# Kernel tuning notes

Hardware: AMD Instinct MI355X
Metric: run time of the kernel (lower is better)

## Reference

```python
import jax, jax.numpy as jnp
import numpy as np

# Standard TCN TemporalBlock (Bai et al.): dilated causal conv -> chomp -> relu ->
# (dropout, identity at eval) x2, plus 1x1-conv residual, final relu.
# PyTorch pads (k-1)*d on both sides then chomps the right, which equals
# left-only causal padding of (k-1)*d.

def _causal_conv(x, w, b, dilation):
    pad = (w.shape[-1] - 1) * dilation
    y = jax.lax.conv_general_dilated(
        x, w, window_strides=(1,), padding=[(pad, 0)],
        rhs_dilation=(dilation,), dimension_numbers=('NCH', 'OIH', 'NCH'))
    return y + b[None, :, None]

def _block(x, w1, b1, w2, b2, wd, bd, dil):
    h = jax.nn.relu(_causal_conv(x, w1, b1, dil))
    h = jax.nn.relu(_causal_conv(h, w2, b2, dil))
    res = _causal_conv(x, wd, bd, 1)  # 1x1 downsample (channel counts differ)
    return jax.nn.relu(h + res)

def setup_inputs() -> dict:
    key = jax.random.key(0)
    ks = jax.random.split(key, 18)
    B, Cin, L, C1, C2, H, K, O = 4096, 30, 256, 100, 200, 8, 5, 1
    def rn(k, shape, s=0.05):
        return jax.random.normal(k, shape, dtype=jnp.float32) * s
    return {
        'x': rn(ks[0], (B, Cin, L), 1.0),
        'task_labels': jax.random.randint(ks[1], (B,), 0, H),
        # TCN level 0: in_features -> 100, dilation 1
        'w1_0': rn(ks[2], (C1, Cin, K)), 'b1_0': rn(ks[3], (C1,)),
        'w2_0': rn(ks[4], (C1, C1, K)),  'b2_0': rn(ks[5], (C1,)),
        'wd_0': rn(ks[6], (C1, Cin, 1)), 'bd_0': rn(ks[7], (C1,)),
        # TCN level 1: 100 -> 200, dilation 2
        'w1_1': rn(ks[8], (C2, C1, K)),  'b1_1': rn(ks[9], (C2,)),
        'w2_1': rn(ks[10], (C2, C2, K)), 'b2_1': rn(ks[11], (C2,)),
        'wd_1': rn(ks[12], (C2, C1, 1)), 'bd_1': rn(ks[13], (C2,)),
        # 8 per-task heads, stacked: Linear(200->100), Tanh, Linear(100->1)
        'hw1': rn(ks[14], (H, C1, C2)), 'hb1': rn(ks[15], (H, C1)),
        'hw2': rn(ks[16], (H, O, C1)),  'hb2': rn(ks[17], (H, O)),
    }

def reference(x, task_labels, w1_0, b1_0, w2_0, b2_0, wd_0, bd_0,
              w1_1, b1_1, w2_1, b2_1, wd_1, bd_1, hw1, hb1, hw2, hb2):
    # TCN backbone (eval mode: dropout is identity)
    y = _block(x, w1_0, b1_0, w2_0, b2_0, wd_0, bd_0, 1)
    y = _block(y, w1_1, b1_1, w2_1, b2_1, wd_1, bd_1, 2)
    feat = y[:, :, -1]  # [B, 200] last timestep
    # Vectorized per-task head dispatch: gather each sample's head weights.
    # Mathematically identical to the per-task gather/MLP/scatter loop.
    W1 = hw1[task_labels]  # [B, 100, 200]
    B1 = hb1[task_labels]  # [B, 100]
    W2 = hw2[task_labels]  # [B, 1, 100]
    B2 = hb2[task_labels]  # [B, 1]
    h = jnp.tanh(jnp.einsum('bd,bod->bo', feat, W1) + B1)
    return jnp.einsum('bo,bpo->bp', h, W2) + B2  # [B, 1]
```

## Files before the change

kernel.cpp:

```cpp
#include <hip/hip_runtime.h>
#include <math.h>


#define B_TOT 4096
#define CIN   30
#define LSEQ  256
#define C1    100
#define C2    200
#define KW    5
#define T0    231
#define WIN   25
#define NT_H0 21
#define NT_Y0 9
#define NT_H1 5

#define NB1 4
__global__ __launch_bounds__(256) void k_h0(const float* __restrict__ x,
                                            const float* __restrict__ w1,
                                            const float* __restrict__ b1,
                                            float* __restrict__ h0) {
  __shared__ float xs[NB1 * CIN * WIN];
  const int b0 = blockIdx.x * NB1;
  const int tid = threadIdx.x;
  for (int idx = tid; idx < NB1 * CIN * WIN; idx += 256) {
    int b = idx / (CIN * WIN);
    int r = idx - b * (CIN * WIN);
    int ci = r / WIN;
    int u = r - ci * WIN;
    xs[idx] = x[(size_t)(b0 + b) * (CIN * LSEQ) + ci * LSEQ + T0 + u];
  }
  __syncthreads();
  const int bl = tid & (NB1 - 1);
  const int cg = tid >> 2;
  const float* xb = xs + bl * (CIN * WIN);
  const int c0 = cg;
  const bool has2 = (cg < C1 - 64);
  const int c1 = has2 ? cg + 64 : cg;

  float acc0[NT_H0], acc1[NT_H0];
  const float bias0 = b1[c0], bias1 = b1[c1];
#pragma unroll
  for (int i = 0; i < NT_H0; ++i) { acc0[i] = bias0; acc1[i] = bias1; }
  const float* wr0 = w1 + c0 * (CIN * KW);
  const float* wr1 = w1 + c1 * (CIN * KW);
  for (int ci = 0; ci < CIN; ++ci) {
    float xr[WIN];
#pragma unroll
    for (int u = 0; u < WIN; ++u) xr[u] = xb[ci * WIN + u];
#pragma unroll
    for (int k = 0; k < KW; ++k) {
      const float wa = wr0[ci * KW + k];
      const float wb = wr1[ci * KW + k];
#pragma unroll
      for (int i = 0; i < NT_H0; ++i) {
        acc0[i] = fmaf(xr[i + k], wa, acc0[i]);
        acc1[i] = fmaf(xr[i + k], wb, acc1[i]);
      }
    }
  }
  float* o0 = h0 + (size_t)(b0 + bl) * (C1 * NT_H0) + c0 * NT_H0;
#pragma unroll
  for (int i = 0; i < NT_H0; ++i) o0[i] = fmaxf(acc0[i], 0.f);
  if (has2) {
    float* o1 = h0 + (size_t)(b0 + bl) * (C1 * NT_H0) + c1 * NT_H0;
#pragma unroll
    for (int i = 0; i < NT_H0; ++i) o1[i] = fmaxf(acc1[i], 0.f);
  }
}

#define NB2 4
__global__ __launch_bounds__(256) void k_y0(const float* __restrict__ x,
                                            const float* __restrict__ h0,
                                            const float* __restrict__ w2,
                                            const float* __restrict__ b2,
                                            const float* __restrict__ wd,
                                            const float* __restrict__ bd,
                                            float* __restrict__ y0) {
  __shared__ float hs[NB2 * C1 * NT_H0];
  __shared__ float xrs[NB2 * CIN * NT_Y0];
  const int b0 = blockIdx.x * NB2;
  const int tid = threadIdx.x;
  for (int idx = tid; idx < NB2 * C1 * NT_H0; idx += 256) {
    int b = idx / (C1 * NT_H0);
    int r = idx - b * (C1 * NT_H0);
    hs[idx] = h0[(size_t)(b0 + b) * (C1 * NT_H0) + r];
  }
  for (int idx = tid; idx < NB2 * CIN * NT_Y0; idx += 256) {
    int b = idx / (CIN * NT_Y0);
    int r = idx - b * (CIN * NT_Y0);
    int ci = r / NT_Y0;
    int j = r - ci * NT_Y0;
    xrs[idx] = x[(size_t)(b0 + b) * (CIN * LSEQ) + ci * LSEQ + T0 + 8 + 2 * j];
  }
  __syncthreads();
  const int bl = tid & (NB2 - 1);
  const int cg = tid >> 2;
  const float* hb = hs + bl * (C1 * NT_H0);
  const float* xb = xrs + bl * (CIN * NT_Y0);
  const int c0 = cg;
  const bool has2 = (cg < C1 - 64);
  const int c1 = has2 ? cg + 64 : cg;

  float acc0[NT_Y0], acc1[NT_Y0];
  const float bA = b2[c0], bB = b2[c1];
#pragma unroll
  for (int j = 0; j < NT_Y0; ++j) { acc0[j] = bA; acc1[j] = bB; }
  const float* wr0 = w2 + c0 * (C1 * KW);
  const float* wr1 = w2 + c1 * (C1 * KW);
  for (int ci = 0; ci < C1; ++ci) {
    float hr[NT_H0];
#pragma unroll
    for (int u = 0; u < NT_H0; ++u) hr[u] = hb[ci * NT_H0 + u];
#pragma unroll
    for (int k = 0; k < KW; ++k) {
      const float wa = wr0[ci * KW + k];
      const float wb = wr1[ci * KW + k];
#pragma unroll
      for (int j = 0; j < NT_Y0; ++j) {
        acc0[j] = fmaf(hr[2 * j + k], wa, acc0[j]);
        acc1[j] = fmaf(hr[2 * j + k], wb, acc1[j]);
      }
    }
  }
  float r0[NT_Y0], r1[NT_Y0];
  const float dA = bd[c0], dB = bd[c1];
#pragma unroll
  for (int j = 0; j < NT_Y0; ++j) { r0[j] = dA; r1[j] = dB; }
  const float* wd0 = wd + c0 * CIN;
  const float* wd1 = wd + c1 * CIN;
  for (int ci = 0; ci < CIN; ++ci) {
    const float wa = wd0[ci], wb = wd1[ci];
#pragma unroll
    for (int j = 0; j < NT_Y0; ++j) {
      const float xv = xb[ci * NT_Y0 + j];
      r0[j] = fmaf(xv, wa, r0[j]);
      r1[j] = fmaf(xv, wb, r1[j]);
    }
  }
  float* o0 = y0 + (size_t)(b0 + bl) * (C1 * NT_Y0) + c0 * NT_Y0;
#pragma unroll
  for (int j = 0; j < NT_Y0; ++j) o0[j] = fmaxf(fmaxf(acc0[j], 0.f) + r0[j], 0.f);
  if (has2) {
    float* o1 = y0 + (size_t)(b0 + bl) * (C1 * NT_Y0) + c1 * NT_Y0;
#pragma unroll
    for (int j = 0; j < NT_Y0; ++j) o1[j] = fmaxf(fmaxf(acc1[j], 0.f) + r1[j], 0.f);
  }
}

#define NB3 4
__global__ __launch_bounds__(256) void k_h1(const float* __restrict__ y0,
                                            const float* __restrict__ w1,
                                            const float* __restrict__ b1,
                                            float* __restrict__ h1) {
  __shared__ float ys[NB3 * C1 * NT_Y0];
  const int b0 = blockIdx.x * NB3;
  const int tid = threadIdx.x;
  for (int idx = tid; idx < NB3 * C1 * NT_Y0; idx += 256) {
    int b = idx / (C1 * NT_Y0);
    int r = idx - b * (C1 * NT_Y0);
    ys[idx] = y0[(size_t)(b0 + b) * (C1 * NT_Y0) + r];
  }
  __syncthreads();
  const int bl = tid & 3;
  const int cg = tid >> 2;
  const float* yb = ys + bl * (C1 * NT_Y0);
  int cidx[4];
  bool valid[4];
#pragma unroll
  for (int m = 0; m < 4; ++m) {
    int c = cg + 64 * m;
    valid[m] = (c < C2);
    cidx[m] = valid[m] ? c : cg;
  }
  float acc[4][NT_H1];
#pragma unroll
  for (int m = 0; m < 4; ++m) {
    const float bb = b1[cidx[m]];
#pragma unroll
    for (int t = 0; t < NT_H1; ++t) acc[m][t] = bb;
  }
  const float* wp[4];
#pragma unroll
  for (int m = 0; m < 4; ++m) wp[m] = w1 + (size_t)cidx[m] * (C1 * KW);
  for (int ci = 0; ci < C1; ++ci) {
    float yr[NT_Y0];
#pragma unroll
    for (int u = 0; u < NT_Y0; ++u) yr[u] = yb[ci * NT_Y0 + u];
#pragma unroll
    for (int k = 0; k < KW; ++k) {
#pragma unroll
      for (int m = 0; m < 4; ++m) {
        const float w = wp[m][ci * KW + k];
#pragma unroll
        for (int t = 0; t < NT_H1; ++t) acc[m][t] = fmaf(yr[t + k], w, acc[m][t]);
      }
    }
  }
#pragma unroll
  for (int m = 0; m < 4; ++m) {
    if (valid[m]) {
      float* o = h1 + (size_t)(b0 + bl) * (C2 * NT_H1) + cidx[m] * NT_H1;
#pragma unroll
      for (int t = 0; t < NT_H1; ++t) o[t] = fmaxf(acc[m][t], 0.f);
    }
  }
}

#define NB4 8
#define NCH4 7
__global__ __launch_bounds__(256) void k_out(const float* __restrict__ y0,
                                             const float* __restrict__ h1,
                                             const float* __restrict__ w2,
                                             const float* __restrict__ b2,
                                             const float* __restrict__ wd,
                                             const float* __restrict__ bd,
                                             const int* __restrict__ labels,
                                             const float* __restrict__ hw1,
                                             const float* __restrict__ hb1,
                                             const float* __restrict__ hw2,
                                             const float* __restrict__ hb2,
                                             float* __restrict__ out) {
  __shared__ float h1s[NB4 * C2 * NT_H1];
  __shared__ float y8s[NB4 * C1];
  __shared__ float feat[NB4 * C2];
  __shared__ float part[32 * NB4];
  const int b0 = blockIdx.x * NB4;
  const int tid = threadIdx.x;
  for (int idx = tid; idx < NB4 * C2 * NT_H1; idx += 256) {
    int b = idx / (C2 * NT_H1);
    int r = idx - b * (C2 * NT_H1);
    h1s[idx] = h1[(size_t)(b0 + b) * (C2 * NT_H1) + r];
  }
  for (int idx = tid; idx < NB4 * C1; idx += 256) {
    int b = idx / C1;
    int c = idx - b * C1;
    y8s[idx] = y0[(size_t)(b0 + b) * (C1 * NT_Y0) + c * NT_Y0 + 8];
  }
  __syncthreads();
  const int bl = tid & (NB4 - 1);
  const int cg = tid >> 3;
  const float* hb = h1s + bl * (C2 * NT_H1);
  const float* yb = y8s + bl * C1;
  int cidx[NCH4];
  bool valid[NCH4];
#pragma unroll
  for (int m = 0; m < NCH4; ++m) {
    int c = cg + 32 * m;
    valid[m] = (c < C2);
    cidx[m] = valid[m] ? c : cg;
  }
  float acc[NCH4];
#pragma unroll
  for (int m = 0; m < NCH4; ++m) acc[m] = b2[cidx[m]];
  for (int cH = 0; cH < C2; ++cH) {
    float h1r[NT_H1];
#pragma unroll
    for (int k = 0; k < NT_H1; ++k) h1r[k] = hb[cH * NT_H1 + k];
#pragma unroll
    for (int m = 0; m < NCH4; ++m) {
      const float* wr = w2 + (size_t)cidx[m] * (C2 * KW) + cH * KW;
#pragma unroll
      for (int k = 0; k < KW; ++k) acc[m] = fmaf(h1r[k], wr[k], acc[m]);
    }
  }
  float rs[NCH4];
#pragma unroll
  for (int m = 0; m < NCH4; ++m) rs[m] = bd[cidx[m]];
  for (int ci = 0; ci < C1; ++ci) {
    const float yv = yb[ci];
#pragma unroll
    for (int m = 0; m < NCH4; ++m) rs[m] = fmaf(yv, wd[cidx[m] * C1 + ci], rs[m]);
  }
#pragma unroll
  for (int m = 0; m < NCH4; ++m) {
    if (valid[m]) feat[bl * C2 + cidx[m]] = fmaxf(fmaxf(acc[m], 0.f) + rs[m], 0.f);
  }
  __syncthreads();
  const int task = labels[b0 + bl];
  const float* fb = feat + bl * C2;
  float p = 0.f;
#pragma unroll
  for (int m = 0; m < 4; ++m) {
    const int o = cg + 32 * m;
    if (o < C1) {
      float a = hb1[task * C1 + o];
      const float* wr = hw1 + (size_t)task * (C1 * C2) + (size_t)o * C2;
      for (int d = 0; d < C2; ++d) a = fmaf(fb[d], wr[d], a);
      p = fmaf(tanhf(a), hw2[task * C1 + o], p);
    }
  }
  part[cg * NB4 + bl] = p;
  __syncthreads();
  if (tid < NB4) {
    const int task2 = labels[b0 + tid];
    float s = hb2[task2];
    for (int g = 0; g < 32; ++g) s += part[g * NB4 + tid];
    out[b0 + tid] = s;
  }
}

extern "C" void kernel_launch(void* const* d_in, const int* in_sizes, int n_in,
                              void* d_out, int out_size, void* d_ws, size_t ws_size,
                              hipStream_t stream) {
  const float* x    = (const float*)d_in[0];
  const int* labels = (const int*)d_in[1];
  const float* w1_0 = (const float*)d_in[2];
  const float* b1_0 = (const float*)d_in[3];
  const float* w2_0 = (const float*)d_in[4];
  const float* b2_0 = (const float*)d_in[5];
  const float* wd_0 = (const float*)d_in[6];
  const float* bd_0 = (const float*)d_in[7];
  const float* w1_1 = (const float*)d_in[8];
  const float* b1_1 = (const float*)d_in[9];
  const float* w2_1 = (const float*)d_in[10];
  const float* b2_1 = (const float*)d_in[11];
  const float* wd_1 = (const float*)d_in[12];
  const float* bd_1 = (const float*)d_in[13];
  const float* hw1  = (const float*)d_in[14];
  const float* hb1  = (const float*)d_in[15];
  const float* hw2  = (const float*)d_in[16];
  const float* hb2  = (const float*)d_in[17];
  float* out = (float*)d_out;

  float* ws = (float*)d_ws;
  float* h0 = ws;
  float* y0 = h0 + (size_t)B_TOT * C1 * NT_H0;
  float* h1 = y0 + (size_t)B_TOT * C1 * NT_Y0;

  hipLaunchKernelGGL(k_h0, dim3(B_TOT / NB1), dim3(256), 0, stream, x, w1_0, b1_0, h0);
  hipLaunchKernelGGL(k_y0, dim3(B_TOT / NB2), dim3(256), 0, stream, x, h0, w2_0, b2_0, wd_0, bd_0, y0);
  hipLaunchKernelGGL(k_h1, dim3(B_TOT / NB3), dim3(256), 0, stream, y0, w1_1, b1_1, h1);
  hipLaunchKernelGGL(k_out, dim3(B_TOT / NB4), dim3(256), 0, stream, y0, h1, w2_1, b2_1,
                     wd_1, bd_1, labels, hw1, hb1, hw2, hb2, out);
}
```

Before: 702.3 us.

## Switch to batch-minor transposed layout with channel-tiled weight-stationary convolutions

Adds a transpose kernel that puts the receptive-field window of x into a batch-minor layout. All intermediates (h0, y0, h1, feat) are stored as [feature][batch], so each lane handles one sample with coalesced loads, while each block stages a channel tile of weights in shared memory and reads them as float4 broadcasts. The final layer is split into a channel-tiled conv plus residual kernel and a separate head kernel that reduces with wave shuffles. The aim is to cut uncoalesced weight reads and make activation traffic coalesced, at the cost of two extra launches and a reused workspace region (h1T overwrites xT).

After: 596.3 us. 15.1% less time.

```diff
diff --git a/kernel.cpp b/kernel.cpp
--- a/kernel.cpp
+++ b/kernel.cpp
@@ -2,7 +2,7 @@
 #include <math.h>
 
 
-#define B_TOT 4096
+#define R     4096
 #define CIN   30
 #define LSEQ  256
 #define C1    100
@@ -10,293 +10,313 @@
 #define KW    5
 #define T0    231
 #define WIN   25
-#define NT_H0 21
-#define NT_Y0 9
-#define NT_H1 5
-
-#define NB1 4
-__global__ __launch_bounds__(256) void k_h0(const float* __restrict__ x,
-                                            const float* __restrict__ w1,
-                                            const float* __restrict__ b1,
-                                            float* __restrict__ h0) {
-  __shared__ float xs[NB1 * CIN * WIN];
-  const int b0 = blockIdx.x * NB1;
-  const int tid = threadIdx.x;
-  for (int idx = tid; idx < NB1 * CIN * WIN; idx += 256) {
-    int b = idx / (CIN * WIN);
-    int r = idx - b * (CIN * WIN);
-    int ci = r / WIN;
-    int u = r - ci * WIN;
-    xs[idx] = x[(size_t)(b0 + b) * (CIN * LSEQ) + ci * LSEQ + T0 + u];
-  }
-  __syncthreads();
-  const int bl = tid & (NB1 - 1);
-  const int cg = tid >> 2;
-  const float* xb = xs + bl * (CIN * WIN);
-  const int c0 = cg;
-  const bool has2 = (cg < C1 - 64);
-  const int c1 = has2 ? cg + 64 : cg;
-
-  float acc0[NT_H0], acc1[NT_H0];
-  const float bias0 = b1[c0], bias1 = b1[c1];
-#pragma unroll
-  for (int i = 0; i < NT_H0; ++i) { acc0[i] = bias0; acc1[i] = bias1; }
-  const float* wr0 = w1 + c0 * (CIN * KW);
-  const float* wr1 = w1 + c1 * (CIN * KW);
+#define NU0   21
+#define NJ0   9
+#define NT1   5
+
+#define ROW_XT    0
+#define ROW_H0T   750
+#define ROW_Y0T   2850
+#define ROW_H1T   0
+#define ROW_FEAT  3750
+
+__global__ __launch_bounds__(1024) void k_tr(const float* __restrict__ x,
+                                             float* __restrict__ xT) {
+  const int l = threadIdx.x & 63;
+  const int wv = threadIdx.x >> 6;
+  const int b = blockIdx.x * 64 + l;
+  const float* xb = x + (size_t)b * (CIN * LSEQ) + T0;
+  for (int r = wv; r < CIN * WIN; r += 16) {
+    const int ci = r / WIN;
+    const int u = r - ci * WIN;
+    xT[(size_t)r * R + b] = xb[ci * LSEQ + u];
+  }
+}
+
+__global__ __launch_bounds__(256) void k1(const float* __restrict__ xT,
+                                          const float* __restrict__ w1,
+                                          const float* __restrict__ b1,
+                                          float* __restrict__ h0T) {
+  __shared__ float wT[CIN * KW * 16];
+  const int tid = threadIdx.x;
+  const int ctile = blockIdx.y * 16;
+  for (int idx = tid; idx < CIN * KW * 16; idx += 256) {
+    const int kk = idx >> 4, cl = idx & 15, c = ctile + cl;
+    wT[idx] = (c < C1) ? w1[c * (CIN * KW) + kk] : 0.f;
+  }
+  __syncthreads();
+  const int l = tid & 63, wv = tid >> 6;
+  const int b = blockIdx.x * 64 + l;
+  const int cb = ctile + wv * 4;
+  float acc[4][NU0];
+#pragma unroll
+  for (int m = 0; m < 4; ++m) {
+    const float bias = (cb + m < C1) ? b1[cb + m] : 0.f;
+#pragma unroll
+    for (int u = 0; u < NU0; ++u) acc[m][u] = bias;
+  }
   for (int ci = 0; ci < CIN; ++ci) {
     float xr[WIN];
-#pragma unroll
-    for (int u = 0; u < WIN; ++u) xr[u] = xb[ci * WIN + u];
+    const float* xp = xT + (size_t)ci * WIN * R + b;
+#pragma unroll
+    for (int u = 0; u < WIN; ++u) xr[u] = xp[(size_t)u * R];
 #pragma unroll
     for (int k = 0; k < KW; ++k) {
-      const float wa = wr0[ci * KW + k];
-      const float wb = wr1[ci * KW + k];
-#pragma unroll
-      for (int i = 0; i < NT_H0; ++i) {
-        acc0[i] = fmaf(xr[i + k], wa, acc0[i]);
-        acc1[i] = fmaf(xr[i + k], wb, acc1[i]);
+      const float4 w = *reinterpret_cast<const float4*>(&wT[(ci * KW + k) * 16 + wv * 4]);
+#pragma unroll
+      for (int u = 0; u < NU0; ++u) {
+        acc[0][u] = fmaf(xr[u + k], w.x, acc[0][u]);
+        acc[1][u] = fmaf(xr[u + k], w.y, acc[1][u]);
+        acc[2][u] = fmaf(xr[u + k], w.z, acc[2][u]);
+        acc[3][u] = fmaf(xr[u + k], w.w, acc[3][u]);
       }
     }
   }
-  float* o0 = h0 + (size_t)(b0 + bl) * (C1 * NT_H0) + c0 * NT_H0;
-#pragma unroll
-  for (int i = 0; i < NT_H0; ++i) o0[i] = fmaxf(acc0[i], 0.f);
-  if (has2) {
-    float* o1 = h0 + (size_t)(b0 + bl) * (C1 * NT_H0) + c1 * NT_H0;
-#pragma unroll
-    for (int i = 0; i < NT_H0; ++i) o1[i] = fmaxf(acc1[i], 0.f);
-  }
-}
-
-#define NB2 4
-__global__ __launch_bounds__(256) void k_y0(const float* __restrict__ x,
-                                            const float* __restrict__ h0,
-                                            const float* __restrict__ w2,
-                                            const float* __restrict__ b2,
-                                            const float* __restrict__ wd,
-                                            const float* __restrict__ bd,
-                                            float* __restrict__ y0) {
-  __shared__ float hs[NB2 * C1 * NT_H0];
-  __shared__ float xrs[NB2 * CIN * NT_Y0];
-  const int b0 = blockIdx.x * NB2;
-  const int tid = threadIdx.x;
-  for (int idx = tid; idx < NB2 * C1 * NT_H0; idx += 256) {
-    int b = idx / (C1 * NT_H0);
-    int r = idx - b * (C1 * NT_H0);
-    hs[idx] = h0[(size_t)(b0 + b) * (C1 * NT_H0) + r];
-  }
-  for (int idx = tid; idx < NB2 * CIN * NT_Y0; idx += 256) {
-    int b = idx / (CIN * NT_Y0);
-    int r = idx - b * (CIN * NT_Y0);
-    int ci = r / NT_Y0;
-    int j = r - ci * NT_Y0;
-    xrs[idx] = x[(size_t)(b0 + b) * (CIN * LSEQ) + ci * LSEQ + T0 + 8 + 2 * j];
-  }
-  __syncthreads();
-  const int bl = tid & (NB2 - 1);
-  const int cg = tid >> 2;
-  const float* hb = hs + bl * (C1 * NT_H0);
-  const float* xb = xrs + bl * (CIN * NT_Y0);
-  const int c0 = cg;
-  const bool has2 = (cg < C1 - 64);
-  const int c1 = has2 ? cg + 64 : cg;
-
-  float acc0[NT_Y0], acc1[NT_Y0];
-  const float bA = b2[c0], bB = b2[c1];
-#pragma unroll
-  for (int j = 0; j < NT_Y0; ++j) { acc0[j] = bA; acc1[j] = bB; }
-  const float* wr0 = w2 + c0 * (C1 * KW);
-  const float* wr1 = w2 + c1 * (C1 * KW);
+#pragma unroll
+  for (int m = 0; m < 4; ++m) {
+    const int c = cb + m;
+    if (c < C1) {
+#pragma unroll
+      for (int u = 0; u < NU0; ++u)
+        h0T[(size_t)(c * NU0 + u) * R + b] = fmaxf(acc[m][u], 0.f);
+    }
+  }
+}
+
+__global__ __launch_bounds__(256) void k2(const float* __restrict__ xT,
+                                          const float* __restrict__ h0T,
+                                          const float* __restrict__ w2,
+                                          const float* __restrict__ b2,
+                                          const float* __restrict__ wd,
+                                          const float* __restrict__ bd,
+                                          float* __restrict__ y0T) {
+  __shared__ float wT[C1 * KW * 16];
+  __shared__ float wdT[CIN * 16];
+  const int tid = threadIdx.x;
+  const int ctile = blockIdx.y * 16;
+  for (int idx = tid; idx < C1 * KW * 16; idx += 256) {
+    const int kk = idx >> 4, cl = idx & 15, c = ctile + cl;
+    wT[idx] = (c < C1) ? w2[c * (C1 * KW) + kk] : 0.f;
+  }
+  for (int idx = tid; idx < CIN * 16; idx += 256) {
+    const int ci = idx >> 4, cl = idx & 15, c = ctile + cl;
+    wdT[idx] = (c < C1) ? wd[c * CIN + ci] : 0.f;
+  }
+  __syncthreads();
+  const int l = tid & 63, wv = tid >> 6;
+  const int b = blockIdx.x * 64 + l;
+  const int cb = ctile + wv * 4;
+  float acc[4][NJ0], rac[4][NJ0];
+#pragma unroll
+  for (int m = 0; m < 4; ++m) {
+    const float bias = (cb + m < C1) ? b2[cb + m] : 0.f;
+    const float bres = (cb + m < C1) ? bd[cb + m] : 0.f;
+#pragma unroll
+    for (int j = 0; j < NJ0; ++j) { acc[m][j] = bias; rac[m][j] = bres; }
+  }
   for (int ci = 0; ci < C1; ++ci) {
-    float hr[NT_H0];
-#pragma unroll
-    for (int u = 0; u < NT_H0; ++u) hr[u] = hb[ci * NT_H0 + u];
+    float hr[NU0];
+    const float* hp = h0T + (size_t)ci * NU0 * R + b;
+#pragma unroll
+    for (int u = 0; u < NU0; ++u) hr[u] = hp[(size_t)u * R];
 #pragma unroll
     for (int k = 0; k < KW; ++k) {
-      const float wa = wr0[ci * KW + k];
-      const float wb = wr1[ci * KW + k];
-#pragma unroll
-      for (int j = 0; j < NT_Y0; ++j) {
-        acc0[j] = fmaf(hr[2 * j + k], wa, acc0[j]);
-        acc1[j] = fmaf(hr[2 * j + k], wb, acc1[j]);
+      const float4 w = *reinterpret_cast<const float4*>(&wT[(ci * KW + k) * 16 + wv * 4]);
+#pragma unroll
+      for (int j = 0; j < NJ0; ++j) {
+        acc[0][j] = fmaf(hr[2 * j + k], w.x, acc[0][j]);
+        acc[1][j] = fmaf(hr[2 * j + k], w.y, acc[1][j]);
+        acc[2][j] = fmaf(hr[2 * j + k], w.z, acc[2][j]);
+        acc[3][j] = fmaf(hr[2 * j + k], w.w, acc[3][j]);
       }
     }
   }
-  float r0[NT_Y0], r1[NT_Y0];
-  const float dA = bd[c0], dB = bd[c1];
-#pragma unroll
-  for (int j = 0; j < NT_Y0; ++j) { r0[j] = dA; r1[j] = dB; }
-  const float* wd0 = wd + c0 * CIN;
-  const float* wd1 = wd + c1 * CIN;
   for (int ci = 0; ci < CIN; ++ci) {
-    const float wa = wd0[ci], wb = wd1[ci];
-#pragma unroll
-    for (int j = 0; j < NT_Y0; ++j) {
-      const float xv = xb[ci * NT_Y0 + j];
-      r0[j] = fmaf(xv, wa, r0[j]);
-      r1[j] = fmaf(xv, wb, r1[j]);
-    }
-  }
-  float* o0 = y0 + (size_t)(b0 + bl) * (C1 * NT_Y0) + c0 * NT_Y0;
-#pragma unroll
-  for (int j = 0; j < NT_Y0; ++j) o0[j] = fmaxf(fmaxf(acc0[j], 0.f) + r0[j], 0.f);
-  if (has2) {
-    float* o1 = y0 + (size_t)(b0 + bl) * (C1 * NT_Y0) + c1 * NT_Y0;
-#pragma unroll
-    for (int j = 0; j < NT_Y0; ++j) o1[j] = fmaxf(fmaxf(acc1[j], 0.f) + r1[j], 0.f);
-  }
-}
-
-#define NB3 4
-__global__ __launch_bounds__(256) void k_h1(const float* __restrict__ y0,
-                                            const float* __restrict__ w1,
-                                            const float* __restrict__ b1,
-                                            float* __restrict__ h1) {
-  __shared__ float ys[NB3 * C1 * NT_Y0];
-  const int b0 = blockIdx.x * NB3;
-  const int tid = threadIdx.x;
-  for (int idx = tid; idx < NB3 * C1 * NT_Y0; idx += 256) {
-    int b = idx / (C1 * NT_Y0);
-    int r = idx - b * (C1 * NT_Y0);
-    ys[idx] = y0[(size_t)(b0 + b) * (C1 * NT_Y0) + r];
-  }
-  __syncthreads();
-  const int bl = tid & 3;
-  const int cg = tid >> 2;
-  const float* yb = ys + bl * (C1 * NT_Y0);
-  int cidx[4];
-  bool valid[4];
-#pragma unroll
-  for (int m = 0; m < 4; ++m) {
-    int c = cg + 64 * m;
-    valid[m] = (c < C2);
-    cidx[m] = valid[m] ? c : cg;
-  }
-  float acc[4][NT_H1];
-#pragma unroll
-  for (int m = 0; m < 4; ++m) {
-    const float bb = b1[cidx[m]];
-#pragma unroll
-    for (int t = 0; t < NT_H1; ++t) acc[m][t] = bb;
-  }
-  const float* wp[4];
-#pragma unroll
-  for (int m = 0; m < 4; ++m) wp[m] = w1 + (size_t)cidx[m] * (C1 * KW);
+    float xr[NJ0];
+    const float* xp = xT + (size_t)(ci * WIN + 8) * R + b;
+#pragma unroll
+    for (int j = 0; j < NJ0; ++j) xr[j] = xp[(size_t)(2 * j) * R];
+    const float4 w = *reinterpret_cast<const float4*>(&wdT[ci * 16 + wv * 4]);
+#pragma unroll
+    for (int j = 0; j < NJ0; ++j) {
+      rac[0][j] = fmaf(xr[j], w.x, rac[0][j]);
+      rac[1][j] = fmaf(xr[j], w.y, rac[1][j]);
+      rac[2][j] = fmaf(xr[j], w.z, rac[2][j]);
+      rac[3][j] = fmaf(xr[j], w.w, rac[3][j]);
+    }
+  }
+#pragma unroll
+  for (int m = 0; m < 4; ++m) {
+    const int c = cb + m;
+    if (c < C1) {
+#pragma unroll
+      for (int j = 0; j < NJ0; ++j)
+        y0T[(size_t)(c * NJ0 + j) * R + b] =
+            fmaxf(fmaxf(acc[m][j], 0.f) + rac[m][j], 0.f);
+    }
+  }
+}
+
+__global__ __launch_bounds__(256) void k3(const float* __restrict__ y0T,
+                                          const float* __restrict__ w1,
+                                          const float* __restrict__ b1,
+                                          float* __restrict__ h1T) {
+  __shared__ float wT[C1 * KW * 16];
+  const int tid = threadIdx.x;
+  const int ctile = blockIdx.y * 16;
+  for (int idx = tid; idx < C1 * KW * 16; idx += 256) {
+    const int kk = idx >> 4, cl = idx & 15, c = ctile + cl;
+    wT[idx] = (c < C2) ? w1[c * (C1 * KW) + kk] : 0.f;
+  }
+  __syncthreads();
+  const int l = tid & 63, wv = tid >> 6;
+  const int b = blockIdx.x * 64 + l;
+  const int cb = ctile + wv * 4;
+  float acc[4][NT1];
+#pragma unroll
+  for (int m = 0; m < 4; ++m) {
+    const float bias = (cb + m < C2) ? b1[cb + m] : 0.f;
+#pragma unroll
+    for (int t = 0; t < NT1; ++t) acc[m][t] = bias;
+  }
   for (int ci = 0; ci < C1; ++ci) {
-    float yr[NT_Y0];
-#pragma unroll
-    for (int u = 0; u < NT_Y0; ++u) yr[u] = yb[ci * NT_Y0 + u];
+    float yr[NJ0];
+    const float* yp = y0T + (size_t)ci * NJ0 * R + b;
+#pragma unroll
+    for (int u = 0; u < NJ0; ++u) yr[u] = yp[(size_t)u * R];
 #pragma unroll
     for (int k = 0; k < KW; ++k) {
-#pragma unroll
-      for (int m = 0; m < 4; ++m) {
-        const float w = wp[m][ci * KW + k];
-#pragma unroll
-        for (int t = 0; t < NT_H1; ++t) acc[m][t] = fmaf(yr[t + k], w, acc[m][t]);
+      const float4 w = *reinterpret_cast<const float4*>(&wT[(ci * KW + k) * 16 + wv * 4]);
+#pragma unroll
+      for (int t = 0; t < NT1; ++t) {
+        acc[0][t] = fmaf(yr[t + k], w.x, acc[0][t]);
+        acc[1][t] = fmaf(yr[t + k], w.y, acc[1][t]);
+        acc[2][t] = fmaf(yr[t + k], w.z, acc[2][t]);
+        acc[3][t] = fmaf(yr[t + k], w.w, acc[3][t]);
       }
     }
   }
 #pragma unroll
   for (int m = 0; m < 4; ++m) {
-    if (valid[m]) {
-      float* o = h1 + (size_t)(b0 + bl) * (C2 * NT_H1) + cidx[m] * NT_H1;
-#pragma unroll
-      for (int t = 0; t < NT_H1; ++t) o[t] = fmaxf(acc[m][t], 0.f);
-    }
-  }
-}
-
-#define NB4 8
-#define NCH4 7
-__global__ __launch_bounds__(256) void k_out(const float* __restrict__ y0,
-                                             const float* __restrict__ h1,
-                                             const float* __restrict__ w2,
-                                             const float* __restrict__ b2,
-                                             const float* __restrict__ wd,
-                                             const float* __restrict__ bd,
-                                             const int* __restrict__ labels,
-                                             const float* __restrict__ hw1,
-                                             const float* __restrict__ hb1,
-                                             const float* __restrict__ hw2,
-                                             const float* __restrict__ hb2,
-                                             float* __restrict__ out) {
-  __shared__ float h1s[NB4 * C2 * NT_H1];
-  __shared__ float y8s[NB4 * C1];
-  __shared__ float feat[NB4 * C2];
-  __shared__ float part[32 * NB4];
-  const int b0 = blockIdx.x * NB4;
-  const int tid = threadIdx.x;
-  for (int idx = tid; idx < NB4 * C2 * NT_H1; idx += 256) {
-    int b = idx / (C2 * NT_H1);
-    int r = idx - b * (C2 * NT_H1);
-    h1s[idx] = h1[(size_t)(b0 + b) * (C2 * NT_H1) + r];
-  }
-  for (int idx = tid; idx < NB4 * C1; idx += 256) {
-    int b = idx / C1;
-    int c = idx - b * C1;
-    y8s[idx] = y0[(size_t)(b0 + b) * (C1 * NT_Y0) + c * NT_Y0 + 8];
-  }
-  __syncthreads();
-  const int bl = tid & (NB4 - 1);
-  const int cg = tid >> 3;
-  const float* hb = h1s + bl * (C2 * NT_H1);
-  const float* yb = y8s + bl * C1;
-  int cidx[NCH4];
-  bool valid[NCH4];
-#pragma unroll
-  for (int m = 0; m < NCH4; ++m) {
-    int c = cg + 32 * m;
-    valid[m] = (c < C2);
-    cidx[m] = valid[m] ? c : cg;
-  }
-  float acc[NCH4];
-#pragma unroll
-  for (int m = 0; m < NCH4; ++m) acc[m] = b2[cidx[m]];
-  for (int cH = 0; cH < C2; ++cH) {
-    float h1r[NT_H1];
-#pragma unroll
-    for (int k = 0; k < NT_H1; ++k) h1r[k] = hb[cH * NT_H1 + k];
-#pragma unroll
-    for (int m = 0; m < NCH4; ++m) {
-      const float* wr = w2 + (size_t)cidx[m] * (C2 * KW) + cH * KW;
-#pragma unroll
-      for (int k = 0; k < KW; ++k) acc[m] = fmaf(h1r[k], wr[k], acc[m]);
-    }
-  }
-  float rs[NCH4];
-#pragma unroll
-  for (int m = 0; m < NCH4; ++m) rs[m] = bd[cidx[m]];
+    const int c = cb + m;
+    if (c < C2) {
+#pragma unroll
+      for (int t = 0; t < NT1; ++t)
+        h1T[(size_t)(c * NT1 + t) * R + b] = fmaxf(acc[m][t], 0.f);
+    }
+  }
+}
+
+__global__ __launch_bounds__(256) void k4a(const float* __restrict__ h1T,
+                                           const float* __restrict__ y0T,
+                                           const float* __restrict__ w2,
+                                           const float* __restrict__ b2,
+                                           const float* __restrict__ wd,
+                                           const float* __restrict__ bd,
+                                           float* __restrict__ featT) {
+  __shared__ float wT[C2 * KW * 8];
+  __shared__ float wdT[C1 * 8];
+  const int tid = threadIdx.x;
+  const int cb8 = blockIdx.y * 8;
+  for (int idx = tid; idx < C2 * KW * 8; idx += 256) {
+    const int kk = idx >> 3, cl = idx & 7;
+    wT[idx] = w2[(cb8 + cl) * (C2 * KW) + kk];
+  }
+  for (int idx = tid; idx < C1 * 8; idx += 256) {
+    const int ci = idx >> 3, cl = idx & 7;
+    wdT[idx] = wd[(cb8 + cl) * C1 + ci];
+  }
+  __syncthreads();
+  const int l = tid & 63, wv = tid >> 6;
+  const int b4 = blockIdx.x * 256 + l * 4;
+  const int c0 = cb8 + wv * 2;
+  float a0[4], a1[4], r0[4], r1[4];
+  {
+    const float bA = b2[c0], bB = b2[c0 + 1];
+    const float dA = bd[c0], dB = bd[c0 + 1];
+#pragma unroll
+    for (int m = 0; m < 4; ++m) { a0[m] = bA; a1[m] = bB; r0[m] = dA; r1[m] = dB; }
+  }
+#pragma unroll 4
+  for (int kk = 0; kk < C2 * KW; ++kk) {
+    const float4 h = *reinterpret_cast<const float4*>(&h1T[(size_t)kk * R + b4]);
+    const float2 w = *reinterpret_cast<const float2*>(&wT[kk * 8 + wv * 2]);
+    a0[0] = fmaf(h.x, w.x, a0[0]); a0[1] = fmaf(h.y, w.x, a0[1]);
+    a0[2] = fmaf(h.z, w.x, a0[2]); a0[3] = fmaf(h.w, w.x, a0[3]);
+    a1[0] = fmaf(h.x, w.y, a1[0]); a1[1] = fmaf(h.y, w.y, a1[1]);
+    a1[2] = fmaf(h.z, w.y, a1[2]); a1[3] = fmaf(h.w, w.y, a1[3]);
+  }
+#pragma unroll 4
   for (int ci = 0; ci < C1; ++ci) {
-    const float yv = yb[ci];
-#pragma unroll
-    for (int m = 0; m < NCH4; ++m) rs[m] = fmaf(yv, wd[cidx[m] * C1 + ci], rs[m]);
-  }
-#pragma unroll
-  for (int m = 0; m < NCH4; ++m) {
-    if (valid[m]) feat[bl * C2 + cidx[m]] = fmaxf(fmaxf(acc[m], 0.f) + rs[m], 0.f);
-  }
-  __syncthreads();
-  const int task = labels[b0 + bl];
-  const float* fb = feat + bl * C2;
+    const float4 y = *reinterpret_cast<const float4*>(&y0T[(size_t)(ci * NJ0 + 8) * R + b4]);
+    const float2 w = *reinterpret_cast<const float2*>(&wdT[ci * 8 + wv * 2]);
+    r0[0] = fmaf(y.x, w.x, r0[0]); r0[1] = fmaf(y.y, w.x, r0[1]);
+    r0[2] = fmaf(y.z, w.x, r0[2]); r0[3] = fmaf(y.w, w.x, r0[3]);
+    r1[0] = fmaf(y.x, w.y, r1[0]); r1[1] = fmaf(y.y, w.y, r1[1]);
+    r1[2] = fmaf(y.z, w.y, r1[2]); r1[3] = fmaf(y.w, w.y, r1[3]);
+  }
+  float4 f0, f1;
+  f0.x = fmaxf(fmaxf(a0[0], 0.f) + r0[0], 0.f);
+  f0.y = fmaxf(fmaxf(a0[1], 0.f) + r0[1], 0.f);
+  f0.z = fmaxf(fmaxf(a0[2], 0.f) + r0[2], 0.f);
+  f0.w = fmaxf(fmaxf(a0[3], 0.f) + r0[3], 0.f);
+  f1.x = fmaxf(fmaxf(a1[0], 0.f) + r1[0], 0.f);
+  f1.y = fmaxf(fmaxf(a1[1], 0.f) + r1[1], 0.f);
+  f1.z = fmaxf(fmaxf(a1[2], 0.f) + r1[2], 0.f);
+  f1.w = fmaxf(fmaxf(a1[3], 0.f) + r1[3], 0.f);
+  *reinterpret_cast<float4*>(&featT[(size_t)c0 * R + b4]) = f0;
+  *reinterpret_cast<float4*>(&featT[(size_t)(c0 + 1) * R + b4]) = f1;
+}
+
+__global__ __launch_bounds__(256) void k4b(const float* __restrict__ featT,
+                                           const int* __restrict__ labels,
+                                           const float* __restrict__ hw1,
+                                           const float* __restrict__ hb1,
+                                           const float* __restrict__ hw2,
+                                           const float* __restrict__ hb2,
+                                           float* __restrict__ out) {
+  __shared__ float fs[4][C2];
+  const int tid = threadIdx.x;
+  const int b0 = blockIdx.x * 4;
+  for (int idx = tid; idx < 4 * C2; idx += 256) {
+    const int c = idx >> 2, bi = idx & 3;
+    fs[bi][c] = featT[(size_t)c * R + b0 + bi];
+  }
+  __syncthreads();
+  const int l = tid & 63, wv = tid >> 6;
+  const int b = b0 + wv;
+  const int task = labels[b];
+  const float* W1 = hw1 + (size_t)task * (C1 * C2);
+  const float* fp = fs[wv];
   float p = 0.f;
-#pragma unroll
-  for (int m = 0; m < 4; ++m) {
-    const int o = cg + 32 * m;
-    if (o < C1) {
-      float a = hb1[task * C1 + o];
-      const float* wr = hw1 + (size_t)task * (C1 * C2) + (size_t)o * C2;
-      for (int d = 0; d < C2; ++d) a = fmaf(fb[d], wr[d], a);
-      p = fmaf(tanhf(a), hw2[task * C1 + o], p);
-    }
-  }
-  part[cg * NB4 + bl] = p;
-  __syncthreads();
-  if (tid < NB4) {
-    const int task2 = labels[b0 + tid];
-    float s = hb2[task2];
-    for (int g = 0; g < 32; ++g) s += part[g * NB4 + tid];
-    out[b0 + tid] = s;
-  }
+  {
+    float a = hb1[task * C1 + l];
+    const float* wr = W1 + (size_t)l * C2;
+#pragma unroll 4
+    for (int d = 0; d < C2; d += 4) {
+      const float4 fv = *reinterpret_cast<const float4*>(&fp[d]);
+      const float4 wv4 = *reinterpret_cast<const float4*>(&wr[d]);
+      a = fmaf(fv.x, wv4.x, a); a = fmaf(fv.y, wv4.y, a);
+      a = fmaf(fv.z, wv4.z, a); a = fmaf(fv.w, wv4.w, a);
+    }
+    p = tanhf(a) * hw2[task * C1 + l];
+  }
+  if (l < C1 - 64) {
+    const int o = 64 + l;
+    float a = hb1[task * C1 + o];
+    const float* wr = W1 + (size_t)o * C2;
+#pragma unroll 4
+    for (int d = 0; d < C2; d += 4) {
+      const float4 fv = *reinterpret_cast<const float4*>(&fp[d]);
+      const float4 wv4 = *reinterpret_cast<const float4*>(&wr[d]);
+      a = fmaf(fv.x, wv4.x, a); a = fmaf(fv.y, wv4.y, a);
+      a = fmaf(fv.z, wv4.z, a); a = fmaf(fv.w, wv4.w, a);
+    }
+    p = fmaf(tanhf(a), hw2[task * C1 + o], p);
+  }
+#pragma unroll
+  for (int off = 32; off > 0; off >>= 1) p += __shfl_down(p, off, 64);
+  if (l == 0) out[b] = p + hb2[task];
 }
 
 extern "C" void kernel_launch(void* const* d_in, const int* in_sizes, int n_in,
@@ -322,14 +342,18 @@
   const float* hb2  = (const float*)d_in[17];
   float* out = (float*)d_out;
 
-  float* ws = (float*)d_ws;
-  float* h0 = ws;
-  float* y0 = h0 + (size_t)B_TOT * C1 * NT_H0;
-  float* h1 = y0 + (size_t)B_TOT * C1 * NT_Y0;
-
-  hipLaunchKernelGGL(k_h0, dim3(B_TOT / NB1), dim3(256), 0, stream, x, w1_0, b1_0, h0);
-  hipLaunchKernelGGL(k_y0, dim3(B_TOT / NB2), dim3(256), 0, stream, x, h0, w2_0, b2_0, wd_0, bd_0, y0);
-  hipLaunchKernelGGL(k_h1, dim3(B_TOT / NB3), dim3(256), 0, stream, y0, w1_1, b1_1, h1);
-  hipLaunchKernelGGL(k_out, dim3(B_TOT / NB4), dim3(256), 0, stream, y0, h1, w2_1, b2_1,
-                     wd_1, bd_1, labels, hw1, hb1, hw2, hb2, out);
-}
+  float* ws    = (float*)d_ws;
+  float* xT    = ws + (size_t)ROW_XT * R;
+  float* h0T   = ws + (size_t)ROW_H0T * R;
+  float* y0T   = ws + (size_t)ROW_Y0T * R;
+  float* h1T   = ws + (size_t)ROW_H1T * R;
+  float* featT = ws + (size_t)ROW_FEAT * R;
+
+  hipLaunchKernelGGL(k_tr, dim3(64), dim3(1024), 0, stream, x, xT);
+  hipLaunchKernelGGL(k1, dim3(64, 7), dim3(256), 0, stream, xT, w1_0, b1_0, h0T);
+  hipLaunchKernelGGL(k2, dim3(64, 7), dim3(256), 0, stream, xT, h0T, w2_0, b2_0, wd_0, bd_0, y0T);
+  hipLaunchKernelGGL(k3, dim3(64, 13), dim3(256), 0, stream, y0T, w1_1, b1_1, h1T);
+  hipLaunchKernelGGL(k4a, dim3(16, 25), dim3(256), 0, stream, h1T, y0T, w2_1, b2_1, wd_1, bd_1, featT);
+  hipLaunchKernelGGL(k4b, dim3(1024), dim3(256), 0, stream, featT, labels,
+                     hw1, hb1, hw2, hb2, out);
+}
```
